# Kernel tuning notes

Hardware: AMD Instinct MI355X
Metric: run time of the kernel (lower is better)

The kernel has to match this reference:

```python
import jax, jax.numpy as jnp
import numpy as np

N, D, T, ET, E = 100000, 128, 3, 4, 250000


def gru_cell(m, h, w_ih, w_hh, b_ih, b_hh):
    # torch.nn.GRUCell semantics
    gi = m @ w_ih.T + b_ih          # [N, 3D]
    gh = h @ w_hh.T + b_hh          # [N, 3D]
    i_r, i_z, i_n = jnp.split(gi, 3, axis=1)
    h_r, h_z, h_n = jnp.split(gh, 3, axis=1)
    r = jax.nn.sigmoid(i_r + h_r)
    z = jax.nn.sigmoid(i_z + h_z)
    n = jnp.tanh(i_n + r * h_n)
    return (1.0 - z) * n + z * h


def setup_inputs() -> dict:
    key = jax.random.key(0)
    ks = jax.random.split(key, 10)
    x = jax.random.normal(ks[0], (N, D), dtype=jnp.float32)
    edge_row = jax.random.randint(ks[1], (ET, E), 0, N, dtype=jnp.int32)
    edge_col = jax.random.randint(ks[2], (ET, E), 0, N, dtype=jnp.int32)
    edge_val = jnp.ones((ET, E), dtype=jnp.float32)
    xav = float(np.sqrt(6.0 / (D + D)))  # xavier_uniform per (D,D) slice
    weight = jax.random.uniform(ks[3], (T, ET, D, D), jnp.float32, -xav, xav)
    bias_w = jax.random.uniform(ks[4], (T, ET, D), jnp.float32, -0.01, 0.01)
    s = float(1.0 / np.sqrt(D))  # GRUCell default init range
    w_ih = jax.random.uniform(ks[5], (3 * D, D), jnp.float32, -s, s)
    w_hh = jax.random.uniform(ks[6], (3 * D, D), jnp.float32, -s, s)
    b_ih = jax.random.uniform(ks[7], (3 * D,), jnp.float32, -s, s)
    b_hh = jax.random.uniform(ks[8], (3 * D,), jnp.float32, -s, s)
    return {"x": x, "edge_row": edge_row, "edge_col": edge_col,
            "edge_val": edge_val, "weight": weight, "bias_w": bias_w,
            "w_ih": w_ih, "w_hh": w_hh, "b_ih": b_ih, "b_hh": b_hh}


def reference(x, edge_row, edge_col, edge_val, weight, bias_w, w_ih, w_hh, b_ih, b_hh):
    n_nodes = x.shape[0]
    h = x  # input_dim == out_channels, no zero-padding needed
    num_t = weight.shape[0]

    def agg_one(m_e, col_e, row_e, val_e):
        # sparse.mm: out[row] += val * m[col]
        msg = m_e[col_e] * val_e[:, None]                 # [E, D]
        return jax.ops.segment_sum(msg, row_e, num_segments=n_nodes)

    for t in range(num_t):
        # per-edge-type dense transform: [ET, N, D]
        m = jnp.einsum('nd,edf->enf', h, weight[t]) + bias_w[t][:, None, :]
        agg = jax.vmap(agg_one)(m, edge_col, edge_row, edge_val)  # [ET, N, D]
        m_sum = agg.sum(axis=0)                                    # [N, D]
        h = gru_cell(m_sum, h, w_ih, w_hh, b_ih, b_hh)
    return h
```

## Files before the change

kernel.cpp:

```cpp
#include <hip/hip_runtime.h>
#include <stdint.h>

#define NN  100000
#define DD  128
#define TT  3
#define ETT 4
#define EE  250000
#define NCH 49
#define GRUGRID 512

typedef float  f32x4  __attribute__((ext_vector_type(4)));
typedef __bf16 bf16x8 __attribute__((ext_vector_type(8)));

__device__ __forceinline__ float bf2f(uint32_t u){ u <<= 16; return __builtin_bit_cast(float, u); }
__device__ __forceinline__ uint32_t f2bf(float f){
  uint32_t u = __builtin_bit_cast(uint32_t, f);
  return (u + 0x7FFFu + ((u >> 16) & 1u)) >> 16;
}
__device__ __forceinline__ f32x4 mfma16(bf16x8 a, bf16x8 b, f32x4 c){
  return __builtin_amdgcn_mfma_f32_16x16x32_bf16(a, b, c, 0, 0, 0);
}

__global__ void k_count(const int* __restrict__ erow, const float* __restrict__ eval,
                        int* __restrict__ counts, float* __restrict__ degval){
  int idx = blockIdx.x * 256 + threadIdx.x;
  if (idx >= ETT * EE) return;
  int e = idx / EE;
  int row = erow[idx];
  atomicAdd(&counts[e * NN + row], 1);
  atomicAdd(&degval[e * NN + row], eval[idx]);
}

__global__ void k_blksum(const int* __restrict__ counts, int* __restrict__ bsum){
  const int b = blockIdx.x, e = b / NCH, c = b % NCH;
  const int* p = counts + e * NN + c * 2048;
  int lim = NN - c * 2048; if (lim > 2048) lim = 2048;
  const int t = threadIdx.x;
  int s = 0;
  #pragma unroll
  for (int i = 0; i < 8; ++i){
    int idx = i * 256 + t;
    if (idx < lim) s += p[idx];
  }
  #pragma unroll
  for (int d = 32; d; d >>= 1) s += __shfl_down(s, d);
  __shared__ int wsum[4];
  if ((t & 63) == 0) wsum[t >> 6] = s;
  __syncthreads();
  if (t == 0) bsum[b] = wsum[0] + wsum[1] + wsum[2] + wsum[3];
}

__global__ void k_scanp(const int* __restrict__ bsum, int* __restrict__ bexc,
                        int* __restrict__ offsets){
  const int t = threadIdx.x, wid = t >> 6, l = t & 63;
  int v = (l < NCH) ? bsum[wid * NCH + l] : 0;
  int x = v;
  #pragma unroll
  for (int d = 1; d < 64; d <<= 1){ int y = __shfl_up(x, d); if (l >= d) x += y; }
  if (l < NCH) bexc[wid * NCH + l] = x - v;
  if (l == NCH - 1) offsets[wid * (NN + 1) + NN] = x;
}

__global__ void k_apply(const int* __restrict__ counts, const int* __restrict__ bexc,
                        int* __restrict__ offsets){
  const int b = blockIdx.x, e = b / NCH, c = b % NCH;
  const int* p = counts + e * NN + c * 2048;
  int* off = offsets + e * (NN + 1) + c * 2048;
  int lim = NN - c * 2048; if (lim > 2048) lim = 2048;
  const int t = threadIdx.x, l = t & 63, wid = t >> 6;
  __shared__ int wt[4];
  int v[8], s = 0;
  #pragma unroll
  for (int i = 0; i < 8; ++i){
    int idx = t * 8 + i;
    v[i] = (idx < lim) ? p[idx] : 0; s += v[i];
  }
  int x = s;
  #pragma unroll
  for (int d = 1; d < 64; d <<= 1){ int y = __shfl_up(x, d); if (l >= d) x += y; }
  if (l == 63) wt[wid] = x;
  __syncthreads();
  int wexc = 0;
  #pragma unroll
  for (int k = 0; k < 4; ++k) if (k < wid) wexc += wt[k];
  int te = bexc[b] + wexc + (x - s);
  #pragma unroll
  for (int i = 0; i < 8; ++i){
    int idx = t * 8 + i;
    if (idx < lim) off[idx] = te;
    te += v[i];
  }
}

__global__ void k_fill(const int* __restrict__ erow, const int* __restrict__ ecol,
                       const float* __restrict__ eval, const int* __restrict__ offsets,
                       int* __restrict__ cursor, uint2* __restrict__ sedge){
  int idx = blockIdx.x * 256 + threadIdx.x;
  if (idx >= ETT * EE) return;
  int e = idx / EE;
  int row = erow[idx];
  int pos = atomicAdd(&cursor[e * NN + row], 1);
  int o = offsets[e * (NN + 1) + row] + pos;
  sedge[e * EE + o] = make_uint2((uint32_t)ecol[idx], __builtin_bit_cast(uint32_t, eval[idx]));
}

__global__ void k_conv_x(const float* __restrict__ x, uint16_t* __restrict__ hbf){
  int idx = blockIdx.x * 256 + threadIdx.x;
  const float4* xp = (const float4*)x;
  float4 a = xp[idx * 2], b = xp[idx * 2 + 1];
  uint32_t p0 = f2bf(a.x) | (f2bf(a.y) << 16);
  uint32_t p1 = f2bf(a.z) | (f2bf(a.w) << 16);
  uint32_t p2 = f2bf(b.x) | (f2bf(b.y) << 16);
  uint32_t p3 = f2bf(b.z) | (f2bf(b.w) << 16);
  ((uint4*)hbf)[idx] = make_uint4(p0, p1, p2, p3);
}

__global__ void k_conv_w(const float* __restrict__ weight, const float* __restrict__ wih,
                         const float* __restrict__ whh, const float* __restrict__ bih,
                         const float* __restrict__ bhh, uint16_t* __restrict__ wcatT,
                         uint16_t* __restrict__ wihb, uint16_t* __restrict__ whhb,
                         float* __restrict__ bcomb){
  int idx = blockIdx.x * 256 + threadIdx.x;
  if (idx < TT * 128 * 512){
    int t = idx / 65536; int rem = idx - t * 65536;
    int f = rem >> 9; int u = rem & 511;
    int e = u >> 7; int d = u & 127;
    wcatT[idx] = (uint16_t)f2bf(weight[(((t * 4 + e) * 128 + d) << 7) + f]);
  }
  if (idx < 384 * 128){
    wihb[idx] = (uint16_t)f2bf(wih[idx]);
    whhb[idx] = (uint16_t)f2bf(whh[idx]);
  }
  if (idx < 256) bcomb[idx] = bih[idx] + bhh[idx];
}

#define ACC8(val, u, base) \
  acc[base+0] += val * bf2f(u.x & 0xffffu); acc[base+1] += val * bf2f(u.x >> 16); \
  acc[base+2] += val * bf2f(u.y & 0xffffu); acc[base+3] += val * bf2f(u.y >> 16); \
  acc[base+4] += val * bf2f(u.z & 0xffffu); acc[base+5] += val * bf2f(u.z >> 16); \
  acc[base+6] += val * bf2f(u.w & 0xffffu); acc[base+7] += val * bf2f(u.w >> 16);

__global__ __launch_bounds__(256, 4) void k_agg_gemm(
    const uint16_t* __restrict__ hbf, const int* __restrict__ offsets,
    const uint2* __restrict__ sedge, const float* __restrict__ degval,
    const float* __restrict__ bias_w, const uint16_t* __restrict__ wcatT_t,
    int tstep, uint16_t* __restrict__ m_out)
{
  __shared__ uint16_t aggT[32 * 512];
  const int tid = threadIdx.x;
  const int node0 = blockIdx.x * 32;

  {
    const int nl = tid >> 3, q = tid & 7;
    const int n = node0 + nl;
    int se[4], ne[4];
    #pragma unroll
    for (int e = 0; e < ETT; ++e){
      se[e] = offsets[e * (NN + 1) + n];
      ne[e] = offsets[e * (NN + 1) + n + 1];
    }
    #pragma unroll 1
    for (int e = 0; e < ETT; ++e){
      float acc[16];
      #pragma unroll
      for (int i = 0; i < 16; ++i) acc[i] = 0.f;
      const int s = se[e], en = ne[e];
      const uint2* ep = sedge + (size_t)e * EE;
      #pragma unroll 1
      for (int i = s; i < en; i += 4){
        const int last = en - 1;
        const int i1 = (i + 1 < last) ? i + 1 : last;
        const int i2 = (i + 2 < last) ? i + 2 : last;
        const int i3 = (i + 3 < last) ? i + 3 : last;
        const uint2 cv0 = ep[i], cv1 = ep[i1], cv2 = ep[i2], cv3 = ep[i3];
        const float v0 = __builtin_bit_cast(float, cv0.y);
        const float v1 = (i + 1 <= last) ? __builtin_bit_cast(float, cv1.y) : 0.f;
        const float v2 = (i + 2 <= last) ? __builtin_bit_cast(float, cv2.y) : 0.f;
        const float v3 = (i + 3 <= last) ? __builtin_bit_cast(float, cv3.y) : 0.f;
        const uint4* p0 = (const uint4*)(hbf + (size_t)cv0.x * DD + q * 16);
        const uint4* p1 = (const uint4*)(hbf + (size_t)cv1.x * DD + q * 16);
        const uint4* p2 = (const uint4*)(hbf + (size_t)cv2.x * DD + q * 16);
        const uint4* p3 = (const uint4*)(hbf + (size_t)cv3.x * DD + q * 16);
        const uint4 a0 = p0[0], b0 = p0[1];
        const uint4 a1 = p1[0], b1 = p1[1];
        const uint4 a2 = p2[0], b2 = p2[1];
        const uint4 a3 = p3[0], b3 = p3[1];
        ACC8(v0, a0, 0); ACC8(v0, b0, 8);
        ACC8(v1, a1, 0); ACC8(v1, b1, 8);
        ACC8(v2, a2, 0); ACC8(v2, b2, 8);
        ACC8(v3, a3, 0); ACC8(v3, b3, 8);
      }
      #pragma unroll
      for (int c2 = 0; c2 < 2; ++c2){
        const int c  = e * 16 + q * 2 + c2;
        const int cs = c ^ (nl & 7);
        uint32_t p0 = f2bf(acc[c2*8+0]) | (f2bf(acc[c2*8+1]) << 16);
        uint32_t p1 = f2bf(acc[c2*8+2]) | (f2bf(acc[c2*8+3]) << 16);
        uint32_t p2 = f2bf(acc[c2*8+4]) | (f2bf(acc[c2*8+5]) << 16);
        uint32_t p3 = f2bf(acc[c2*8+6]) | (f2bf(acc[c2*8+7]) << 16);
        *(uint4*)&aggT[nl * 512 + cs * 8] = make_uint4(p0, p1, p2, p3);
      }
    }
  }
  __syncthreads();

  const int lane = tid & 63, w = tid >> 6;
  const int rlo = lane & 15, kg = lane >> 4;
  const int rt = w & 1, fh = w >> 1;
  const int rowA = rt * 16 + rlo;
  f32x4 C[4];
  #pragma unroll
  for (int i = 0; i < 4; ++i) C[i] = f32x4{0.f, 0.f, 0.f, 0.f};

  #pragma unroll
  for (int ks = 0; ks < 16; ++ks){
    const int cs = (ks * 4 + kg) ^ (rowA & 7);
    bf16x8 a = __builtin_bit_cast(bf16x8, *(const uint4*)&aggT[rowA * 512 + cs * 8]);
    #pragma unroll
    for (int ft = 0; ft < 4; ++ft){
      const int f = fh * 64 + ft * 16 + rlo;
      bf16x8 b = __builtin_bit_cast(bf16x8, *(const uint4*)(wcatT_t + (size_t)f * 512 + ks * 32 + kg * 8));
      C[ft] = mfma16(a, b, C[ft]);
    }
  }

  const float* bwt = bias_w + tstep * (ETT * DD);
  float dv[4][4];
  #pragma unroll
  for (int r = 0; r < 4; ++r){
    const int n2 = node0 + rt * 16 + kg * 4 + r;
    #pragma unroll
    for (int e = 0; e < 4; ++e) dv[e][r] = degval[e * NN + n2];
  }
  #pragma unroll
  for (int ft = 0; ft < 4; ++ft){
    const int f = fh * 64 + ft * 16 + rlo;
    const float b0 = bwt[f], b1 = bwt[128 + f], b2 = bwt[256 + f], b3 = bwt[384 + f];
    #pragma unroll
    for (int r = 0; r < 4; ++r){
      const int n2 = node0 + rt * 16 + kg * 4 + r;
      const float bias = dv[0][r]*b0 + dv[1][r]*b1 + dv[2][r]*b2 + dv[3][r]*b3;
      m_out[(size_t)n2 * DD + f] = (uint16_t)f2bf(C[ft][r] + bias);
    }
  }
}

__global__ __launch_bounds__(512, 2) void k_gru(
    const uint16_t* __restrict__ m_sum, const uint16_t* __restrict__ hsrc,
    uint16_t* __restrict__ hdst, const float* __restrict__ h_old,
    float* __restrict__ h_new, const uint16_t* __restrict__ wihb,
    const uint16_t* __restrict__ whhb, const float* __restrict__ bcomb,
    const float* __restrict__ b_ih, const float* __restrict__ b_hh)
{
  __shared__ uint4 mt[2][512];
  __shared__ uint4 ht[2][512];
  const int tid = threadIdx.x;
  const int lane = tid & 63, w = tid >> 6;
  const int rlo = lane & 15, kg = lane >> 4;

  bf16x8 wa[3][4], wb[3][4];
  #pragma unroll
  for (int g = 0; g < 3; ++g){
    const int j = g * 128 + w * 16 + rlo;
    #pragma unroll
    for (int ks = 0; ks < 4; ++ks){
      wa[g][ks] = __builtin_bit_cast(bf16x8, *(const uint4*)(wihb + j * 128 + ks * 32 + kg * 8));
      wb[g][ks] = __builtin_bit_cast(bf16x8, *(const uint4*)(whhb + j * 128 + ks * 32 + kg * 8));
    }
  }
  const int d0 = w * 16 + kg * 4;
  const f32x4 brz = *(const f32x4*)(bcomb + d0);
  const f32x4 bzz = *(const f32x4*)(bcomb + 128 + d0);
  const f32x4 bin = *(const f32x4*)(b_ih + 256 + d0);
  const f32x4 bhn = *(const f32x4*)(b_hh + 256 + d0);

  const int sn  = tid >> 4;
  const int scs = tid & 15;
  const int sc  = scs ^ (sn & 7);

  const int NT = NN / 32;
  int tile = blockIdx.x;
  {
    const size_t base = ((size_t)(tile * 32 + sn)) * DD + sc * 8;
    mt[0][sn * 16 + scs] = *(const uint4*)(m_sum + base);
    ht[0][sn * 16 + scs] = *(const uint4*)(hsrc + base);
  }
  __syncthreads();

  int buf = 0;
  #pragma unroll 1
  for (; tile < NT; tile += GRUGRID){
    const int ntile = tile + GRUGRID;
    const bool have = ntile < NT;
    uint4 mv, hv;
    if (have){
      const size_t nbase = ((size_t)(ntile * 32 + sn)) * DD + sc * 8;
      mv = *(const uint4*)(m_sum + nbase);
      hv = *(const uint4*)(hsrc + nbase);
    }

    f32x4 acc[3][2][2];
    #pragma unroll
    for (int g = 0; g < 3; ++g)
      #pragma unroll
      for (int m = 0; m < 2; ++m)
        #pragma unroll
        for (int ns = 0; ns < 2; ++ns) acc[g][m][ns] = f32x4{0.f,0.f,0.f,0.f};

    #pragma unroll
    for (int ks = 0; ks < 4; ++ks){
      #pragma unroll
      for (int ns = 0; ns < 2; ++ns){
        const int node = ns * 16 + rlo;
        const int cs = (ks * 4 + kg) ^ (node & 7);
        const bf16x8 bm = __builtin_bit_cast(bf16x8, mt[buf][node * 16 + cs]);
        const bf16x8 bh = __builtin_bit_cast(bf16x8, ht[buf][node * 16 + cs]);
        #pragma unroll
        for (int g = 0; g < 3; ++g){
          acc[g][0][ns] = mfma16(wa[g][ks], bm, acc[g][0][ns]);
          acc[g][1][ns] = mfma16(wb[g][ks], bh, acc[g][1][ns]);
        }
      }
    }

    #pragma unroll
    for (int ns = 0; ns < 2; ++ns){
      const int node = tile * 32 + ns * 16 + rlo;
      const f32x4 ho = *(const f32x4*)(h_old + (size_t)node * DD + d0);
      float hvv[4];
      #pragma unroll
      for (int r = 0; r < 4; ++r){
        const float rg = 1.f / (1.f + __expf(-(acc[0][0][ns][r] + acc[0][1][ns][r] + brz[r])));
        const float zg = 1.f / (1.f + __expf(-(acc[1][0][ns][r] + acc[1][1][ns][r] + bzz[r])));
        const float xa = (acc[2][0][ns][r] + bin[r]) + rg * (acc[2][1][ns][r] + bhn[r]);
        const float ng = 1.f - 2.f / (__expf(2.f * xa) + 1.f);
        hvv[r] = (1.f - zg) * ng + zg * ho[r];
      }
      *(f32x4*)(h_new + (size_t)node * DD + d0) = f32x4{hvv[0], hvv[1], hvv[2], hvv[3]};
      uint32_t p0 = f2bf(hvv[0]) | (f2bf(hvv[1]) << 16);
      uint32_t p1 = f2bf(hvv[2]) | (f2bf(hvv[3]) << 16);
      *(uint2*)(hdst + (size_t)node * DD + d0) = make_uint2(p0, p1);
    }

    if (have){
      mt[buf ^ 1][sn * 16 + scs] = mv;
      ht[buf ^ 1][sn * 16 + scs] = hv;
    }
    __syncthreads();
    buf ^= 1;
  }
}

extern "C" void kernel_launch(void* const* d_in, const int* in_sizes, int n_in,
                              void* d_out, int out_size, void* d_ws, size_t ws_size,
                              hipStream_t stream) {
  const float* x      = (const float*)d_in[0];
  const int*   erow   = (const int*)d_in[1];
  const int*   ecol   = (const int*)d_in[2];
  const float* eval   = (const float*)d_in[3];
  const float* weight = (const float*)d_in[4];
  const float* bias_w = (const float*)d_in[5];
  const float* wih    = (const float*)d_in[6];
  const float* whh    = (const float*)d_in[7];
  const float* bih    = (const float*)d_in[8];
  const float* bhh    = (const float*)d_in[9];
  float* out = (float*)d_out;
  char* ws = (char*)d_ws;

  size_t o = 0;
  auto alloc = [&](size_t bytes)->char*{ char* p = ws + o; o += (bytes + 255) & ~(size_t)255; return p; };
  int*      counts  = (int*)     alloc((size_t)ETT * NN * 4);
  int*      cursor  = (int*)     alloc((size_t)ETT * NN * 4);
  float*    degval  = (float*)   alloc((size_t)ETT * NN * 4);
  int*      offsets = (int*)     alloc((size_t)ETT * (NN + 1) * 4);
  int*      bsum    = (int*)     alloc((size_t)ETT * NCH * 4);
  int*      bexc    = (int*)     alloc((size_t)ETT * NCH * 4);
  uint2*    sedge   = (uint2*)   alloc((size_t)ETT * EE * 8);
  float*    hf      = (float*)   alloc((size_t)NN * DD * 4);
  uint16_t* hbf0    = (uint16_t*)alloc((size_t)NN * DD * 2);
  uint16_t* hbf1    = (uint16_t*)alloc((size_t)NN * DD * 2);
  uint16_t* msum    = (uint16_t*)alloc((size_t)NN * DD * 2);
  uint16_t* wcatT   = (uint16_t*)alloc((size_t)TT * 128 * 512 * 2);
  uint16_t* wihb    = (uint16_t*)alloc((size_t)384 * 128 * 2);
  uint16_t* whhb    = (uint16_t*)alloc((size_t)384 * 128 * 2);
  float*    bcomb   = (float*)   alloc((size_t)256 * 4);
  (void)ws_size; (void)in_sizes; (void)n_in; (void)out_size;

  hipMemsetAsync(counts, 0, (size_t)3 * ETT * NN * 4, stream);

  k_count<<<(ETT * EE + 255) / 256, 256, 0, stream>>>(erow, eval, counts, degval);
  k_blksum<<<ETT * NCH, 256, 0, stream>>>(counts, bsum);
  k_scanp<<<1, 256, 0, stream>>>(bsum, bexc, offsets);
  k_apply<<<ETT * NCH, 256, 0, stream>>>(counts, bexc, offsets);
  k_fill<<<(ETT * EE + 255) / 256, 256, 0, stream>>>(erow, ecol, eval, offsets, cursor, sedge);
  k_conv_x<<<(NN * DD / 8) / 256, 256, 0, stream>>>(x, hbf0);
  k_conv_w<<<(TT * 128 * 512 + 255) / 256, 256, 0, stream>>>(weight, wih, whh, bih, bhh,
                                                             wcatT, wihb, whhb, bcomb);

  uint16_t* hsrc = hbf0;
  uint16_t* hdst = hbf1;
  for (int t = 0; t < TT; ++t){
    k_agg_gemm<<<NN / 32, 256, 0, stream>>>(hsrc, offsets, sedge, degval,
                                            bias_w, wcatT + (size_t)t * 65536, t, msum);
    const float* hold = (t == 0) ? x : hf;
    float* hnew = (t == TT - 1) ? out : hf;
    k_gru<<<GRUGRID, 512, 0, stream>>>(msum, hsrc, hdst, hold, hnew,
                                       wihb, whhb, bcomb, bih, bhh);
    uint16_t* tmp = hsrc; hsrc = hdst; hdst = tmp;
  }
}
```

Before: 721.4 us.

## Halve nodes per block in fused aggregate-GEMM, use 16 lanes per node

The fused aggregation+GEMM kernel now handles 16 nodes per block instead of 32. Each node gets 16 threads that each gather one 16-byte chunk per edge instead of two, and each wave computes a 16x32 output tile. The accumulator state per thread is halved, LDS use drops to 16 KB, and launch bounds allow 8 blocks per CU, aiming for more memory-level parallelism on the irregular gathers. The cost is that each block's 256x128 weight slab is loaded by twice as many blocks, and each MFMA A-fragment is reused across fewer output tiles.

```diff
diff --git a/kernel.cpp b/kernel.cpp
--- a/kernel.cpp
+++ b/kernel.cpp
@@ -134,37 +134,32 @@
   if (idx < 256) bcomb[idx] = bih[idx] + bhh[idx];
 }
 
-#define ACC8(val, u, base) \
-  acc[base+0] += val * bf2f(u.x & 0xffffu); acc[base+1] += val * bf2f(u.x >> 16); \
-  acc[base+2] += val * bf2f(u.y & 0xffffu); acc[base+3] += val * bf2f(u.y >> 16); \
-  acc[base+4] += val * bf2f(u.z & 0xffffu); acc[base+5] += val * bf2f(u.z >> 16); \
-  acc[base+6] += val * bf2f(u.w & 0xffffu); acc[base+7] += val * bf2f(u.w >> 16);
-
-__global__ __launch_bounds__(256, 4) void k_agg_gemm(
+#define ACC8(val, u) \
+  acc[0] += val * bf2f(u.x & 0xffffu); acc[1] += val * bf2f(u.x >> 16); \
+  acc[2] += val * bf2f(u.y & 0xffffu); acc[3] += val * bf2f(u.y >> 16); \
+  acc[4] += val * bf2f(u.z & 0xffffu); acc[5] += val * bf2f(u.z >> 16); \
+  acc[6] += val * bf2f(u.w & 0xffffu); acc[7] += val * bf2f(u.w >> 16);
+
+__global__ __launch_bounds__(256, 8) void k_agg_gemm(
     const uint16_t* __restrict__ hbf, const int* __restrict__ offsets,
     const uint2* __restrict__ sedge, const float* __restrict__ degval,
     const float* __restrict__ bias_w, const uint16_t* __restrict__ wcatT_t,
     int tstep, uint16_t* __restrict__ m_out)
 {
-  __shared__ uint16_t aggT[32 * 512];
+  __shared__ uint16_t aggT[16 * 512];
   const int tid = threadIdx.x;
-  const int node0 = blockIdx.x * 32;
+  const int node0 = blockIdx.x * 16;
 
   {
-    const int nl = tid >> 3, q = tid & 7;
+    const int nl = tid >> 4, q = tid & 15;
     const int n = node0 + nl;
-    int se[4], ne[4];
-    #pragma unroll
-    for (int e = 0; e < ETT; ++e){
-      se[e] = offsets[e * (NN + 1) + n];
-      ne[e] = offsets[e * (NN + 1) + n + 1];
-    }
     #pragma unroll 1
     for (int e = 0; e < ETT; ++e){
-      float acc[16];
+      float acc[8];
       #pragma unroll
-      for (int i = 0; i < 16; ++i) acc[i] = 0.f;
-      const int s = se[e], en = ne[e];
+      for (int i = 0; i < 8; ++i) acc[i] = 0.f;
+      const int s  = offsets[e * (NN + 1) + n];
+      const int en = offsets[e * (NN + 1) + n + 1];
       const uint2* ep = sedge + (size_t)e * EE;
       #pragma unroll 1
       for (int i = s; i < en; i += 4){
@@ -177,48 +172,36 @@
         const float v1 = (i + 1 <= last) ? __builtin_bit_cast(float, cv1.y) : 0.f;
         const float v2 = (i + 2 <= last) ? __builtin_bit_cast(float, cv2.y) : 0.f;
         const float v3 = (i + 3 <= last) ? __builtin_bit_cast(float, cv3.y) : 0.f;
-        const uint4* p0 = (const uint4*)(hbf + (size_t)cv0.x * DD + q * 16);
-        const uint4* p1 = (const uint4*)(hbf + (size_t)cv1.x * DD + q * 16);
-        const uint4* p2 = (const uint4*)(hbf + (size_t)cv2.x * DD + q * 16);
-        const uint4* p3 = (const uint4*)(hbf + (size_t)cv3.x * DD + q * 16);
-        const uint4 a0 = p0[0], b0 = p0[1];
-        const uint4 a1 = p1[0], b1 = p1[1];
-        const uint4 a2 = p2[0], b2 = p2[1];
-        const uint4 a3 = p3[0], b3 = p3[1];
-        ACC8(v0, a0, 0); ACC8(v0, b0, 8);
-        ACC8(v1, a1, 0); ACC8(v1, b1, 8);
-        ACC8(v2, a2, 0); ACC8(v2, b2, 8);
-        ACC8(v3, a3, 0); ACC8(v3, b3, 8);
+        const uint4 u0 = *(const uint4*)(hbf + (size_t)cv0.x * DD + q * 8);
+        const uint4 u1 = *(const uint4*)(hbf + (size_t)cv1.x * DD + q * 8);
+        const uint4 u2 = *(const uint4*)(hbf + (size_t)cv2.x * DD + q * 8);
+        const uint4 u3 = *(const uint4*)(hbf + (size_t)cv3.x * DD + q * 8);
+        ACC8(v0, u0); ACC8(v1, u1); ACC8(v2, u2); ACC8(v3, u3);
       }
-      #pragma unroll
-      for (int c2 = 0; c2 < 2; ++c2){
-        const int c  = e * 16 + q * 2 + c2;
-        const int cs = c ^ (nl & 7);
-        uint32_t p0 = f2bf(acc[c2*8+0]) | (f2bf(acc[c2*8+1]) << 16);
-        uint32_t p1 = f2bf(acc[c2*8+2]) | (f2bf(acc[c2*8+3]) << 16);
-        uint32_t p2 = f2bf(acc[c2*8+4]) | (f2bf(acc[c2*8+5]) << 16);
-        uint32_t p3 = f2bf(acc[c2*8+6]) | (f2bf(acc[c2*8+7]) << 16);
-        *(uint4*)&aggT[nl * 512 + cs * 8] = make_uint4(p0, p1, p2, p3);
-      }
+      const int c  = e * 16 + q;
+      const int cs = c ^ (nl & 7);
+      uint32_t p0 = f2bf(acc[0]) | (f2bf(acc[1]) << 16);
+      uint32_t p1 = f2bf(acc[2]) | (f2bf(acc[3]) << 16);
+      uint32_t p2 = f2bf(acc[4]) | (f2bf(acc[5]) << 16);
+      uint32_t p3 = f2bf(acc[6]) | (f2bf(acc[7]) << 16);
+      *(uint4*)&aggT[nl * 512 + cs * 8] = make_uint4(p0, p1, p2, p3);
     }
   }
   __syncthreads();
 
   const int lane = tid & 63, w = tid >> 6;
   const int rlo = lane & 15, kg = lane >> 4;
-  const int rt = w & 1, fh = w >> 1;
-  const int rowA = rt * 16 + rlo;
-  f32x4 C[4];
-  #pragma unroll
-  for (int i = 0; i < 4; ++i) C[i] = f32x4{0.f, 0.f, 0.f, 0.f};
+  f32x4 C[2];
+  C[0] = f32x4{0.f, 0.f, 0.f, 0.f};
+  C[1] = f32x4{0.f, 0.f, 0.f, 0.f};
 
   #pragma unroll
   for (int ks = 0; ks < 16; ++ks){
-    const int cs = (ks * 4 + kg) ^ (rowA & 7);
-    bf16x8 a = __builtin_bit_cast(bf16x8, *(const uint4*)&aggT[rowA * 512 + cs * 8]);
-    #pragma unroll
-    for (int ft = 0; ft < 4; ++ft){
-      const int f = fh * 64 + ft * 16 + rlo;
+    const int cs = (ks * 4 + kg) ^ (rlo & 7);
+    bf16x8 a = __builtin_bit_cast(bf16x8, *(const uint4*)&aggT[rlo * 512 + cs * 8]);
+    #pragma unroll
+    for (int ft = 0; ft < 2; ++ft){
+      const int f = w * 32 + ft * 16 + rlo;
       bf16x8 b = __builtin_bit_cast(bf16x8, *(const uint4*)(wcatT_t + (size_t)f * 512 + ks * 32 + kg * 8));
       C[ft] = mfma16(a, b, C[ft]);
     }
@@ -228,17 +211,17 @@
   float dv[4][4];
   #pragma unroll
   for (int r = 0; r < 4; ++r){
-    const int n2 = node0 + rt * 16 + kg * 4 + r;
+    const int n2 = node0 + kg * 4 + r;
     #pragma unroll
     for (int e = 0; e < 4; ++e) dv[e][r] = degval[e * NN + n2];
   }
   #pragma unroll
-  for (int ft = 0; ft < 4; ++ft){
-    const int f = fh * 64 + ft * 16 + rlo;
+  for (int ft = 0; ft < 2; ++ft){
+    const int f = w * 32 + ft * 16 + rlo;
     const float b0 = bwt[f], b1 = bwt[128 + f], b2 = bwt[256 + f], b3 = bwt[384 + f];
     #pragma unroll
     for (int r = 0; r < 4; ++r){
-      const int n2 = node0 + rt * 16 + kg * 4 + r;
+      const int n2 = node0 + kg * 4 + r;
       const float bias = dv[0][r]*b0 + dv[1][r]*b1 + dv[2][r]*b2 + dv[3][r]*b3;
       m_out[(size_t)n2 * DD + f] = (uint16_t)f2bf(C[ft][r] + bias);
     }
@@ -400,7 +383,7 @@
   uint16_t* hsrc = hbf0;
   uint16_t* hdst = hbf1;
   for (int t = 0; t < TT; ++t){
-    k_agg_gemm<<<NN / 32, 256, 0, stream>>>(hsrc, offsets, sedge, degval,
+    k_agg_gemm<<<NN / 16, 256, 0, stream>>>(hsrc, offsets, sedge, degval,
                                             bias_w, wcatT + (size_t)t * 65536, t, msum);
     const float* hold = (t == 0) ? x : hf;
     float* hnew = (t == TT - 1) ? out : hf;
```

New measurement: 753.8 us. 4.5% more time.

## Fuse aggregation-GEMM and GRU cell into one per-step kernel

Applied to the files above, without the earlier changes.

Merges the aggregation+edge-type GEMM kernel with the GRU kernel so each 32-node block keeps its message tile in shared memory and runs the GRU matmuls directly. This removes the bf16 m_sum round trip through global memory and one launch per step. GRU weights are pre-packed into MFMA fragment order and read from global/L2 per block rather than held in registers across a persistent loop. The cost is more per-block weight traffic, higher register pressure in the fused kernel, and no load overlap in the GRU phase.

```diff
diff --git a/kernel.cpp b/kernel.cpp
--- a/kernel.cpp
+++ b/kernel.cpp
@@ -7,7 +7,6 @@
 #define ETT 4
 #define EE  250000
 #define NCH 49
-#define GRUGRID 512
 
 typedef float  f32x4  __attribute__((ext_vector_type(4)));
 typedef __bf16 bf16x8 __attribute__((ext_vector_type(8)));
@@ -118,8 +117,7 @@
 __global__ void k_conv_w(const float* __restrict__ weight, const float* __restrict__ wih,
                          const float* __restrict__ whh, const float* __restrict__ bih,
                          const float* __restrict__ bhh, uint16_t* __restrict__ wcatT,
-                         uint16_t* __restrict__ wihb, uint16_t* __restrict__ whhb,
-                         float* __restrict__ bcomb){
+                         uint16_t* __restrict__ wgru, float* __restrict__ bcomb){
   int idx = blockIdx.x * 256 + threadIdx.x;
   if (idx < TT * 128 * 512){
     int t = idx / 65536; int rem = idx - t * 65536;
@@ -127,9 +125,16 @@
     int e = u >> 7; int d = u & 127;
     wcatT[idx] = (uint16_t)f2bf(weight[(((t * 4 + e) * 128 + d) << 7) + f]);
   }
-  if (idx < 384 * 128){
-    wihb[idx] = (uint16_t)f2bf(wih[idx]);
-    whhb[idx] = (uint16_t)f2bf(whh[idx]);
+  if (idx < 192 * 512){
+    const int frag = idx >> 9, within = idx & 511;
+    const int lane = within >> 3, i = within & 7;
+    const int ks = frag & 3, bb = (frag >> 2) & 1, m = (frag >> 3) & 1;
+    const int rem2 = frag >> 4;
+    const int g = rem2 % 3, w = rem2 / 3;
+    const int j = g * 128 + w * 32 + bb * 16 + (lane & 15);
+    const int k = ks * 32 + (lane >> 4) * 8 + i;
+    const float* src = m ? whh : wih;
+    wgru[idx] = (uint16_t)f2bf(src[j * 128 + k]);
   }
   if (idx < 256) bcomb[idx] = bih[idx] + bhh[idx];
 }
@@ -140,13 +145,17 @@
   acc[base+4] += val * bf2f(u.z & 0xffffu); acc[base+5] += val * bf2f(u.z >> 16); \
   acc[base+6] += val * bf2f(u.w & 0xffffu); acc[base+7] += val * bf2f(u.w >> 16);
 
-__global__ __launch_bounds__(256, 4) void k_agg_gemm(
-    const uint16_t* __restrict__ hbf, const int* __restrict__ offsets,
-    const uint2* __restrict__ sedge, const float* __restrict__ degval,
-    const float* __restrict__ bias_w, const uint16_t* __restrict__ wcatT_t,
-    int tstep, uint16_t* __restrict__ m_out)
+__global__ __launch_bounds__(256, 4) void k_step(
+    const uint16_t* __restrict__ hsrc, uint16_t* __restrict__ hdst,
+    const float* __restrict__ h_old, float* __restrict__ h_new,
+    const int* __restrict__ offsets, const uint2* __restrict__ sedge,
+    const float* __restrict__ degval, const float* __restrict__ bias_w,
+    const uint16_t* __restrict__ wcatT_t, int tstep,
+    const uint16_t* __restrict__ wgru, const float* __restrict__ bcomb,
+    const float* __restrict__ b_ih, const float* __restrict__ b_hh)
 {
   __shared__ uint16_t aggT[32 * 512];
+  __shared__ uint4 hT4[512];
   const int tid = threadIdx.x;
   const int node0 = blockIdx.x * 32;
 
@@ -177,10 +186,10 @@
         const float v1 = (i + 1 <= last) ? __builtin_bit_cast(float, cv1.y) : 0.f;
         const float v2 = (i + 2 <= last) ? __builtin_bit_cast(float, cv2.y) : 0.f;
         const float v3 = (i + 3 <= last) ? __builtin_bit_cast(float, cv3.y) : 0.f;
-        const uint4* p0 = (const uint4*)(hbf + (size_t)cv0.x * DD + q * 16);
-        const uint4* p1 = (const uint4*)(hbf + (size_t)cv1.x * DD + q * 16);
-        const uint4* p2 = (const uint4*)(hbf + (size_t)cv2.x * DD + q * 16);
-        const uint4* p3 = (const uint4*)(hbf + (size_t)cv3.x * DD + q * 16);
+        const uint4* p0 = (const uint4*)(hsrc + (size_t)cv0.x * DD + q * 16);
+        const uint4* p1 = (const uint4*)(hsrc + (size_t)cv1.x * DD + q * 16);
+        const uint4* p2 = (const uint4*)(hsrc + (size_t)cv2.x * DD + q * 16);
+        const uint4* p3 = (const uint4*)(hsrc + (size_t)cv3.x * DD + q * 16);
         const uint4 a0 = p0[0], b0 = p0[1];
         const uint4 a1 = p1[0], b1 = p1[1];
         const uint4 a2 = p2[0], b2 = p2[1];
@@ -206,6 +215,15 @@
 
   const int lane = tid & 63, w = tid >> 6;
   const int rlo = lane & 15, kg = lane >> 4;
+
+  #pragma unroll
+  for (int i = 0; i < 2; ++i){
+    const int slot = tid * 2 + i;
+    const int sn = slot >> 4, scs = slot & 15;
+    const int sc = scs ^ (sn & 7);
+    hT4[slot] = *(const uint4*)(hsrc + (size_t)(node0 + sn) * DD + sc * 8);
+  }
+
   const int rt = w & 1, fh = w >> 1;
   const int rowA = rt * 16 + rlo;
   f32x4 C[4];
@@ -232,73 +250,25 @@
     #pragma unroll
     for (int e = 0; e < 4; ++e) dv[e][r] = degval[e * NN + n2];
   }
+  __syncthreads();
+
+  uint16_t* mT = aggT;
   #pragma unroll
   for (int ft = 0; ft < 4; ++ft){
     const int f = fh * 64 + ft * 16 + rlo;
     const float b0 = bwt[f], b1 = bwt[128 + f], b2 = bwt[256 + f], b3 = bwt[384 + f];
     #pragma unroll
     for (int r = 0; r < 4; ++r){
-      const int n2 = node0 + rt * 16 + kg * 4 + r;
+      const int n2l = rt * 16 + kg * 4 + r;
       const float bias = dv[0][r]*b0 + dv[1][r]*b1 + dv[2][r]*b2 + dv[3][r]*b3;
-      m_out[(size_t)n2 * DD + f] = (uint16_t)f2bf(C[ft][r] + bias);
-    }
-  }
-}
-
-__global__ __launch_bounds__(512, 2) void k_gru(
-    const uint16_t* __restrict__ m_sum, const uint16_t* __restrict__ hsrc,
-    uint16_t* __restrict__ hdst, const float* __restrict__ h_old,
-    float* __restrict__ h_new, const uint16_t* __restrict__ wihb,
-    const uint16_t* __restrict__ whhb, const float* __restrict__ bcomb,
-    const float* __restrict__ b_ih, const float* __restrict__ b_hh)
-{
-  __shared__ uint4 mt[2][512];
-  __shared__ uint4 ht[2][512];
-  const int tid = threadIdx.x;
-  const int lane = tid & 63, w = tid >> 6;
-  const int rlo = lane & 15, kg = lane >> 4;
-
-  bf16x8 wa[3][4], wb[3][4];
-  #pragma unroll
-  for (int g = 0; g < 3; ++g){
-    const int j = g * 128 + w * 16 + rlo;
-    #pragma unroll
-    for (int ks = 0; ks < 4; ++ks){
-      wa[g][ks] = __builtin_bit_cast(bf16x8, *(const uint4*)(wihb + j * 128 + ks * 32 + kg * 8));
-      wb[g][ks] = __builtin_bit_cast(bf16x8, *(const uint4*)(whhb + j * 128 + ks * 32 + kg * 8));
-    }
-  }
-  const int d0 = w * 16 + kg * 4;
-  const f32x4 brz = *(const f32x4*)(bcomb + d0);
-  const f32x4 bzz = *(const f32x4*)(bcomb + 128 + d0);
-  const f32x4 bin = *(const f32x4*)(b_ih + 256 + d0);
-  const f32x4 bhn = *(const f32x4*)(b_hh + 256 + d0);
-
-  const int sn  = tid >> 4;
-  const int scs = tid & 15;
-  const int sc  = scs ^ (sn & 7);
-
-  const int NT = NN / 32;
-  int tile = blockIdx.x;
-  {
-    const size_t base = ((size_t)(tile * 32 + sn)) * DD + sc * 8;
-    mt[0][sn * 16 + scs] = *(const uint4*)(m_sum + base);
-    ht[0][sn * 16 + scs] = *(const uint4*)(hsrc + base);
-  }
-  __syncthreads();
-
-  int buf = 0;
-  #pragma unroll 1
-  for (; tile < NT; tile += GRUGRID){
-    const int ntile = tile + GRUGRID;
-    const bool have = ntile < NT;
-    uint4 mv, hv;
-    if (have){
-      const size_t nbase = ((size_t)(ntile * 32 + sn)) * DD + sc * 8;
-      mv = *(const uint4*)(m_sum + nbase);
-      hv = *(const uint4*)(hsrc + nbase);
-    }
-
+      mT[n2l * 128 + (((f >> 3) ^ (n2l & 7)) << 3) + (f & 7)] = (uint16_t)f2bf(C[ft][r] + bias);
+    }
+  }
+  __syncthreads();
+
+  const uint4* mT4 = (const uint4*)aggT;
+  #pragma unroll
+  for (int bb = 0; bb < 2; ++bb){
     f32x4 acc[3][2][2];
     #pragma unroll
     for (int g = 0; g < 3; ++g)
@@ -309,45 +279,51 @@
 
     #pragma unroll
     for (int ks = 0; ks < 4; ++ks){
+      bf16x8 fa[3], fb[3];
+      #pragma unroll
+      for (int g = 0; g < 3; ++g){
+        const int fragA = (((w * 3 + g) * 2 + 0) * 2 + bb) * 4 + ks;
+        const int fragB = (((w * 3 + g) * 2 + 1) * 2 + bb) * 4 + ks;
+        fa[g] = __builtin_bit_cast(bf16x8, *(const uint4*)(wgru + fragA * 512 + lane * 8));
+        fb[g] = __builtin_bit_cast(bf16x8, *(const uint4*)(wgru + fragB * 512 + lane * 8));
+      }
       #pragma unroll
       for (int ns = 0; ns < 2; ++ns){
         const int node = ns * 16 + rlo;
         const int cs = (ks * 4 + kg) ^ (node & 7);
-        const bf16x8 bm = __builtin_bit_cast(bf16x8, mt[buf][node * 16 + cs]);
-        const bf16x8 bh = __builtin_bit_cast(bf16x8, ht[buf][node * 16 + cs]);
+        const bf16x8 bm = __builtin_bit_cast(bf16x8, mT4[node * 16 + cs]);
+        const bf16x8 bh = __builtin_bit_cast(bf16x8, hT4[node * 16 + cs]);
         #pragma unroll
         for (int g = 0; g < 3; ++g){
-          acc[g][0][ns] = mfma16(wa[g][ks], bm, acc[g][0][ns]);
-          acc[g][1][ns] = mfma16(wb[g][ks], bh, acc[g][1][ns]);
+          acc[g][0][ns] = mfma16(fa[g], bm, acc[g][0][ns]);
+          acc[g][1][ns] = mfma16(fb[g], bh, acc[g][1][ns]);
         }
       }
     }
 
+    const int d0 = w * 32 + bb * 16 + kg * 4;
+    const f32x4 brz = *(const f32x4*)(bcomb + d0);
+    const f32x4 bzz = *(const f32x4*)(bcomb + 128 + d0);
+    const f32x4 bin = *(const f32x4*)(b_ih + 256 + d0);
+    const f32x4 bhn = *(const f32x4*)(b_hh + 256 + d0);
     #pragma unroll
     for (int ns = 0; ns < 2; ++ns){
-      const int node = tile * 32 + ns * 16 + rlo;
+      const int node = node0 + ns * 16 + rlo;
       const f32x4 ho = *(const f32x4*)(h_old + (size_t)node * DD + d0);
-      float hvv[4];
+      float hv[4];
       #pragma unroll
       for (int r = 0; r < 4; ++r){
         const float rg = 1.f / (1.f + __expf(-(acc[0][0][ns][r] + acc[0][1][ns][r] + brz[r])));
         const float zg = 1.f / (1.f + __expf(-(acc[1][0][ns][r] + acc[1][1][ns][r] + bzz[r])));
         const float xa = (acc[2][0][ns][r] + bin[r]) + rg * (acc[2][1][ns][r] + bhn[r]);
         const float ng = 1.f - 2.f / (__expf(2.f * xa) + 1.f);
-        hvv[r] = (1.f - zg) * ng + zg * ho[r];
-      }
-      *(f32x4*)(h_new + (size_t)node * DD + d0) = f32x4{hvv[0], hvv[1], hvv[2], hvv[3]};
-      uint32_t p0 = f2bf(hvv[0]) | (f2bf(hvv[1]) << 16);
-      uint32_t p1 = f2bf(hvv[2]) | (f2bf(hvv[3]) << 16);
+        hv[r] = (1.f - zg) * ng + zg * ho[r];
+      }
+      *(f32x4*)(h_new + (size_t)node * DD + d0) = f32x4{hv[0], hv[1], hv[2], hv[3]};
+      uint32_t p0 = f2bf(hv[0]) | (f2bf(hv[1]) << 16);
+      uint32_t p1 = f2bf(hv[2]) | (f2bf(hv[3]) << 16);
       *(uint2*)(hdst + (size_t)node * DD + d0) = make_uint2(p0, p1);
     }
-
-    if (have){
-      mt[buf ^ 1][sn * 16 + scs] = mv;
-      ht[buf ^ 1][sn * 16 + scs] = hv;
-    }
-    __syncthreads();
-    buf ^= 1;
   }
 }
 
@@ -379,10 +355,8 @@
   float*    hf      = (float*)   alloc((size_t)NN * DD * 4);
   uint16_t* hbf0    = (uint16_t*)alloc((size_t)NN * DD * 2);
   uint16_t* hbf1    = (uint16_t*)alloc((size_t)NN * DD * 2);
-  uint16_t* msum    = (uint16_t*)alloc((size_t)NN * DD * 2);
   uint16_t* wcatT   = (uint16_t*)alloc((size_t)TT * 128 * 512 * 2);
-  uint16_t* wihb    = (uint16_t*)alloc((size_t)384 * 128 * 2);
-  uint16_t* whhb    = (uint16_t*)alloc((size_t)384 * 128 * 2);
+  uint16_t* wgru    = (uint16_t*)alloc((size_t)192 * 512 * 2);
   float*    bcomb   = (float*)   alloc((size_t)256 * 4);
   (void)ws_size; (void)in_sizes; (void)n_in; (void)out_size;
 
@@ -395,17 +369,16 @@
   k_fill<<<(ETT * EE + 255) / 256, 256, 0, stream>>>(erow, ecol, eval, offsets, cursor, sedge);
   k_conv_x<<<(NN * DD / 8) / 256, 256, 0, stream>>>(x, hbf0);
   k_conv_w<<<(TT * 128 * 512 + 255) / 256, 256, 0, stream>>>(weight, wih, whh, bih, bhh,
-                                                             wcatT, wihb, whhb, bcomb);
-
-  uint16_t* hsrc = hbf0;
-  uint16_t* hdst = hbf1;
+                                                             wcatT, wgru, bcomb);
+
+  uint16_t* hs = hbf0;
+  uint16_t* hd = hbf1;
   for (int t = 0; t < TT; ++t){
-    k_agg_gemm<<<NN / 32, 256, 0, stream>>>(hsrc, offsets, sedge, degval,
-                                            bias_w, wcatT + (size_t)t * 65536, t, msum);
     const float* hold = (t == 0) ? x : hf;
     float* hnew = (t == TT - 1) ? out : hf;
-    k_gru<<<GRUGRID, 512, 0, stream>>>(msum, hsrc, hdst, hold, hnew,
-                                       wihb, whhb, bcomb, bih, bhh);
-    uint16_t* tmp = hsrc; hsrc = hdst; hdst = tmp;
-  }
-}
+    k_step<<<NN / 32, 256, 0, stream>>>(hs, hd, hold, hnew, offsets, sedge, degval,
+                                        bias_w, wcatT + (size_t)t * 65536, t,
+                                        wgru, bcomb, bih, bhh);
+    uint16_t* tmp = hs; hs = hd; hd = tmp;
+  }
+}
```

Measured after the change: 721.0 us. Within noise of the previous version (-0.1%).
